# Kernel tuning notes

Measured on AMD Instinct MI355X. Metric: run time of the kernel, lower is better.

The kernel has to match this reference:

```python
import jax, jax.numpy as jnp
import numpy as np

AC_KERNEL = 5


def deconv(x, w, stride):
    """torch ConvTranspose2d(k=3, p=1, bias=False), stride 1 or 2 (output_padding=1).
    w has torch layout [Cin, Cout, kH, kW]."""
    wk = jnp.transpose(w, (1, 0, 2, 3))[:, :, ::-1, ::-1]  # OIHW, spatially flipped
    dn = ('NCHW', 'OIHW', 'NCHW')
    if stride == 1:
        return jax.lax.conv_general_dilated(x, wk, (1, 1), ((1, 1), (1, 1)), dimension_numbers=dn)
    # stride 2: dilate input, pad (k-1-p, k-1-p+op) = (1, 2) -> doubles H, W
    return jax.lax.conv_general_dilated(x, wk, (1, 1), ((1, 2), (1, 2)),
                                        lhs_dilation=(2, 2), dimension_numbers=dn)


def sepconv(feat, kv, kh, K):
    """Per-pixel adaptive separable convolution (Niklaus SepConv).
    feat: [B,C,H,W]; kv, kh: [B,K,H,W]. Replication-pad by K//2, then
    out[b,c,y,x] = sum_{i,j} pad[b,c,y+i,x+j] * kv[b,i,y,x] * kh[b,j,y,x]."""
    pad = K // 2
    B, C, H, W = feat.shape
    p = jnp.pad(feat, ((0, 0), (0, 0), (pad, pad), (pad, pad)), mode='edge')
    out = jnp.zeros_like(feat)
    for i in range(K):  # small fixed loop over kernel taps
        row = p[:, :, i:i + H, :]  # [B,C,H,W+2*pad]
        horiz = row[:, :, :, 0:W] * kh[:, 0:1]
        for j in range(1, K):
            horiz = horiz + row[:, :, :, j:j + W] * kh[:, j:j + 1]
        out = out + kv[:, i:i + 1] * horiz
    return out


def fusion(feat, kv, kh, mask):
    tmp = sepconv(feat, kv, kh, AC_KERNEL)
    return mask * tmp + (1.0 - mask) * feat


def setup_inputs() -> dict:
    key = jax.random.key(0)
    ks = jax.random.split(key, 20)
    B, G = 128, 64
    d = {'cont_feat': jax.random.normal(ks[0], (B, G, 8, 8), jnp.float32)}
    sizes = [8, 16, 32, 64]
    for li, s in enumerate(sizes):
        d[f'kv{li}'] = jax.random.uniform(ks[1 + 3 * li], (B, AC_KERNEL, s, s), jnp.float32)
        d[f'kh{li}'] = jax.random.uniform(ks[2 + 3 * li], (B, AC_KERNEL, s, s), jnp.float32)
        d[f'm{li}'] = jax.random.uniform(ks[3 + 3 * li], (B, 1, s, s), jnp.float32)
    wshapes = [(G, G * 8, 3, 3), (G * 8, G * 4, 3, 3), (G * 4, G * 2, 3, 3),
               (G * 2, G * 2, 3, 3), (G * 2, G, 3, 3), (G, 3, 3, 3)]
    for wi, ws in enumerate(wshapes):
        d[f'w{wi + 1}'] = jax.random.normal(ks[13 + wi], ws, jnp.float32) * 0.05
    return d


def reference(cont_feat, kv0, kh0, m0, kv1, kh1, m1, kv2, kh2, m2, kv3, kh3, m3,
              w1, w2, w3, w4, w5, w6):
    # kernel_layer = 4, no_mask = False, use_bn = False
    feat_8 = fusion(cont_feat, kv0, kh0, m0)                      # [B,G,8,8]
    feat_16 = jax.nn.relu(deconv(feat_8, w1, 2))                  # [B,8G,16,16]
    feat_16 = fusion(feat_16, kv1, kh1, m1)
    h = jax.nn.relu(deconv(feat_16, w2, 1))                       # [B,4G,16,16]
    feat_32 = jax.nn.relu(deconv(h, w3, 2))                       # [B,2G,32,32]
    feat_32 = fusion(feat_32, kv2, kh2, m2)
    h = jax.nn.relu(deconv(feat_32, w4, 1))                       # [B,2G,32,32]
    h = jax.nn.relu(deconv(h, w5, 2))                             # [B,G,64,64]
    out = jnp.tanh(deconv(h, w6, 1))                              # [B,3,64,64]
    out = fusion(out, kv3, kh3, m3)
    return (out, feat_8, feat_16, feat_32)
```

## Files before the change

kernel.cpp:

```cpp
#include <hip/hip_runtime.h>
#include <math.h>

typedef short v8s __attribute__((ext_vector_type(8)));
typedef float v16f __attribute__((ext_vector_type(16)));

__device__ inline unsigned short f2bf(float f) {
    union { float f; unsigned u; } c; c.f = f;
    unsigned r = (c.u + 0x7fffu + ((c.u >> 16) & 1u)) >> 16;
    return (unsigned short)r;
}

__global__ __launch_bounds__(256) void fusion_kernel(
        const float* __restrict__ feat, const float* __restrict__ kv,
        const float* __restrict__ kh, const float* __restrict__ m,
        float* __restrict__ out, int C, int H, int W, int total) {
    int idx = blockIdx.x * 256 + threadIdx.x;
    if (idx >= total) return;
    int x = idx % W;
    int y = (idx / W) % H;
    int b = idx / (W * H * C);
    int hw = H * W;
    int pix = y * W + x;
    float mv = m[b * hw + pix];
    float kvv[5], khv[5];
#pragma unroll
    for (int i = 0; i < 5; i++) {
        kvv[i] = kv[(b * 5 + i) * hw + pix];
        khv[i] = kh[(b * 5 + i) * hw + pix];
    }
    int cx[5], cy[5];
#pragma unroll
    for (int j = 0; j < 5; j++) {
        int xx = x + j - 2; cx[j] = xx < 0 ? 0 : (xx >= W ? W - 1 : xx);
        int yy = y + j - 2; cy[j] = yy < 0 ? 0 : (yy >= H ? H - 1 : yy);
    }
    const float* fp = feat + (size_t)(idx - pix);
    float s = 0.f;
#pragma unroll
    for (int i = 0; i < 5; i++) {
        const float* rp = fp + cy[i] * W;
        float h = 0.f;
#pragma unroll
        for (int j = 0; j < 5; j++) h += rp[cx[j]] * khv[j];
        s += kvv[i] * h;
    }
    float fv = feat[idx];
    out[idx] = mv * s + (1.f - mv) * fv;
}

__global__ __launch_bounds__(256) void nchw_to_nhwc_bf16(
        const float* __restrict__ in, unsigned short* __restrict__ out,
        int C, int H, int W, int lw, int lc2) {
    extern __shared__ unsigned short sm_t[];
    const int y = blockIdx.x, b = blockIdx.y;
    const int Cp = C + 8;
    const int tid = threadIdx.x;
    for (int i = tid; i < C * W; i += 256) {
        int x = i & (W - 1), c = i >> lw;
        float v = in[(((size_t)b * C + c) * H + y) * W + x];
        sm_t[x * Cp + c] = f2bf(v);
    }
    __syncthreads();
    const unsigned* s32 = (const unsigned*)sm_t;
    unsigned* o32 = (unsigned*)(out + (((size_t)b * H + y) * W) * C);
    const int n32 = (W * C) >> 1;
    for (int i = tid; i < n32; i += 256) {
        int x = i >> lc2;
        int c2 = i - (x << lc2);
        o32[i] = s32[x * (Cp >> 1) + c2];
    }
}

__global__ __launch_bounds__(256) void repack_w_frag(
        const float* __restrict__ w, unsigned short* __restrict__ wk,
        int Cin, int Cout, int flip) {
    int idx = blockIdx.x * 256 + threadIdx.x;
    if (idx >= Cin * Cout) return;
    int ci = idx / Cout, co = idx - ci * Cout;
    const float* src = w + (size_t)idx * 9;
    const int nCb = Cout >> 5, nH = Cin >> 4;
    const size_t inner = (size_t)((((ci >> 3) & 1) * 32 + (co & 31)) * 8 + (ci & 7));
#pragma unroll
    for (int k = 0; k < 9; k++) {
        int t = flip ? (8 - k) : k;
        size_t blk = ((size_t)t * nCb + (co >> 5)) * nH + (ci >> 4);
        wk[(blk << 9) + inner] = f2bf(src[k]);
    }
}

template<int W, int TH, int LW>
__global__ __launch_bounds__(256) void conv3x3_mfma(
        const unsigned short* __restrict__ X,
        const unsigned short* __restrict__ Wk,
        unsigned short* __restrict__ out, int Cin, int Cout, int H) {
    constexpr int TP = (TH + 2) * (W + 2);
    __shared__ unsigned short sB[TP * 40];
    const int tid = threadIdx.x;
    const int lane = tid & 63, wv = tid >> 6;
    const int wm = wv >> 1, wn = wv & 1;
    const int y0 = blockIdx.x * TH;
    const int coB = blockIdx.y * 128 + wm * 64;
    const int b = blockIdx.z;
    const int n = lane & 31, kg = lane >> 5;
    const int p0 = wn * 64 + n, p1 = p0 + 32;
    const int r0 = p0 >> LW, c0 = p0 & (W - 1);
    const int r1 = p1 >> LW, c1 = p1 & (W - 1);
    const int bo0 = (r0 * (W + 2) + c0) * 40 + kg * 8;
    const int bo1 = (r1 * (W + 2) + c1) * 40 + kg * 8;
    v16f acc00 = {}, acc01 = {}, acc10 = {}, acc11 = {};
    const size_t cbStride = (size_t)(Cin >> 4) << 9;
    const size_t tStride  = (size_t)(Cout >> 5) * cbStride;
    const unsigned short* Af = Wk + (size_t)(coB >> 5) * cbStride + (lane << 3);
    const unsigned short* Xb = X + (size_t)b * H * W * Cin;

    for (int ci0 = 0; ci0 < Cin; ci0 += 32) {
        for (int i = tid; i < TP * 4; i += 256) {
            int pix = i >> 2, part = i & 3;
            int py = pix / (W + 2), px = pix - py * (W + 2);
            int gy = y0 + py - 1, gx = px - 1;
            uint4 v = make_uint4(0u, 0u, 0u, 0u);
            if (gy >= 0 && gy < H && (unsigned)gx < (unsigned)W)
                v = *(const uint4*)(Xb + ((size_t)(gy * W + gx)) * Cin + ci0 + part * 8);
            *(uint4*)(sB + pix * 40 + part * 8) = v;
        }
        __syncthreads();
#pragma unroll
        for (int t = 0; t < 9; t++) {
            const int ky = t / 3, kx = t - ky * 3;
            const int toff = (ky * (W + 2) + kx) * 40;
#pragma unroll
            for (int kh = 0; kh < 2; kh++) {
                const unsigned short* ap =
                    Af + (size_t)t * tStride + (size_t)(((ci0 >> 4) + kh) << 9);
                v8s A0 = *(const v8s*)(ap);
                v8s A1 = *(const v8s*)(ap + cbStride);
                v8s B0 = *(const v8s*)(sB + bo0 + toff + kh * 16);
                v8s B1 = *(const v8s*)(sB + bo1 + toff + kh * 16);
                acc00 = __builtin_amdgcn_mfma_f32_32x32x16_bf16(A0, B0, acc00, 0, 0, 0);
                acc01 = __builtin_amdgcn_mfma_f32_32x32x16_bf16(A0, B1, acc01, 0, 0, 0);
                acc10 = __builtin_amdgcn_mfma_f32_32x32x16_bf16(A1, B0, acc10, 0, 0, 0);
                acc11 = __builtin_amdgcn_mfma_f32_32x32x16_bf16(A1, B1, acc11, 0, 0, 0);
            }
        }
        __syncthreads();
    }
    unsigned short* ob = out + (size_t)b * H * W * Cout;
#pragma unroll
    for (int sm = 0; sm < 2; sm++) {
        v16f a0 = sm ? acc10 : acc00;
        v16f a1 = sm ? acc11 : acc01;
        const int cobase = coB + sm * 32 + 4 * kg;
        unsigned short* q0p = ob + ((size_t)((y0 + r0) * W + c0)) * Cout + cobase;
        unsigned short* q1p = ob + ((size_t)((y0 + r1) * W + c1)) * Cout + cobase;
#pragma unroll
        for (int r2 = 0; r2 < 4; r2++) {
            ushort4 q0, q1; float v;
            v = a0[4 * r2 + 0]; v = v > 0.f ? v : 0.f; q0.x = f2bf(v);
            v = a0[4 * r2 + 1]; v = v > 0.f ? v : 0.f; q0.y = f2bf(v);
            v = a0[4 * r2 + 2]; v = v > 0.f ? v : 0.f; q0.z = f2bf(v);
            v = a0[4 * r2 + 3]; v = v > 0.f ? v : 0.f; q0.w = f2bf(v);
            *(ushort4*)(q0p + 8 * r2) = q0;
            v = a1[4 * r2 + 0]; v = v > 0.f ? v : 0.f; q1.x = f2bf(v);
            v = a1[4 * r2 + 1]; v = v > 0.f ? v : 0.f; q1.y = f2bf(v);
            v = a1[4 * r2 + 2]; v = v > 0.f ? v : 0.f; q1.z = f2bf(v);
            v = a1[4 * r2 + 3]; v = v > 0.f ? v : 0.f; q1.w = f2bf(v);
            *(ushort4*)(q1p + 8 * r2) = q1;
        }
    }
}

template<int W, int TH, int NWN, int NWM, int LW>
__global__ __launch_bounds__(256) void deconv2_mfma(
        const unsigned short* __restrict__ X,
        const unsigned short* __restrict__ Wk,
        float* __restrict__ out, int Cin, int Cout, int Hin) {
    constexpr int ROWS = NWN * TH + 1;
    constexpr int NPIX = ROWS * (W + 1);
    __shared__ unsigned short sB[NPIX * 40];
    const int tid = threadIdx.x;
    const int lane = tid & 63, wv = tid >> 6;
    const int wm = wv / NWN, wn = wv % NWN;
    const int n = lane & 31, kg = lane >> 5;
    const int y0 = blockIdx.x * (NWN * TH);
    const int coB = (blockIdx.y * NWM + wm) * 64;
    const int b = blockIdx.z;
    const int Yl = wn * TH + (n >> LW);
    const int Xl = n & (W - 1);
    v16f zero = {};
    v16f acc[2][2][2];
#pragma unroll
    for (int i = 0; i < 2; i++)
#pragma unroll
        for (int j = 0; j < 2; j++)
#pragma unroll
            for (int s = 0; s < 2; s++) acc[i][j][s] = zero;
    const unsigned short* Xb = X + (size_t)b * Hin * W * Cin;
    const size_t cbStride = (size_t)(Cin >> 4) << 9;
    const size_t tStride  = (size_t)(Cout >> 5) * cbStride;
    const unsigned short* Af = Wk + (size_t)(coB >> 5) * cbStride + (lane << 3);
    const int PY[3] = {1, 0, 1}, DY[3] = {1, 0, 0};

    for (int ci0 = 0; ci0 < Cin; ci0 += 32) {
        for (int i = tid; i < NPIX * 4; i += 256) {
            int pix = i >> 2, part = i & 3;
            int py_ = pix / (W + 1), px_ = pix - py_ * (W + 1);
            int gy = y0 + py_, gx = px_;
            uint4 v = make_uint4(0u, 0u, 0u, 0u);
            if (gy < Hin && gx < W)
                v = *(const uint4*)(Xb + ((size_t)(gy * W + gx)) * Cin + ci0 + part * 8);
            *(uint4*)(sB + pix * 40 + part * 8) = v;
        }
        __syncthreads();
#pragma unroll
        for (int ky = 0; ky < 3; ky++) {
#pragma unroll
            for (int kx = 0; kx < 3; kx++) {
                const int py = PY[ky], dy = DY[ky];
                const int px = PY[kx], dx = DY[kx];
                const int t = ky * 3 + kx;
                const int boff = ((Yl + dy) * (W + 1) + (Xl + dx)) * 40 + kg * 8;
#pragma unroll
                for (int kh = 0; kh < 2; kh++) {
                    const unsigned short* ap =
                        Af + (size_t)t * tStride + (size_t)(((ci0 >> 4) + kh) << 9);
                    v8s B  = *(const v8s*)(sB + boff + kh * 16);
                    v8s A0 = *(const v8s*)(ap);
                    v8s A1 = *(const v8s*)(ap + cbStride);
                    acc[py][px][0] = __builtin_amdgcn_mfma_f32_32x32x16_bf16(A0, B, acc[py][px][0], 0, 0, 0);
                    acc[py][px][1] = __builtin_amdgcn_mfma_f32_32x32x16_bf16(A1, B, acc[py][px][1], 0, 0, 0);
                }
            }
        }
        __syncthreads();
    }
    const int Wo = 2 * W, Ho = 2 * Hin;
    const int yin = y0 + Yl;
#pragma unroll
    for (int py = 0; py < 2; py++) {
        const int oy = 2 * yin + py;
#pragma unroll
        for (int sm = 0; sm < 2; sm++) {
            const int cobase = coB + sm * 32 + 4 * kg;
#pragma unroll
            for (int r = 0; r < 16; r++) {
                int co = cobase + (r & 3) + 8 * (r >> 2);
                float v0 = acc[py][0][sm][r]; v0 = v0 > 0.f ? v0 : 0.f;
                float v1 = acc[py][1][sm][r]; v1 = v1 > 0.f ? v1 : 0.f;
                *(float2*)(out + (((size_t)(b * Cout + co) * Ho + oy) * Wo + 2 * Xl)) =
                    make_float2(v0, v1);
            }
        }
    }
}

__global__ __launch_bounds__(256) void conv_s1_c3_tanh_kernel(
        const float* __restrict__ in, const float* __restrict__ w,
        float* __restrict__ out, int Cin, int H, int W) {
    __shared__ float sIn[8][18][19];
    __shared__ float sW[8][3][9];
    const int tid = threadIdx.x;
    const int r = tid >> 4, c = tid & 15;
    const int ntx = W >> 4;
    const int tx0 = (blockIdx.x % ntx) << 4, ty0 = (blockIdx.x / ntx) << 4;
    const int b = blockIdx.z;
    const int hw = H * W;
    float acc[3] = {0.f, 0.f, 0.f};
    for (int ci0 = 0; ci0 < Cin; ci0 += 8) {
        for (int i = tid; i < 8 * 18 * 18; i += 256) {
            int ci = i / 324, rr = i % 324, ly = rr / 18, lx = rr % 18;
            int gy = ty0 + ly - 1, gx = tx0 + lx - 1;
            float v = 0.f;
            if (gy >= 0 && gy < H && gx >= 0 && gx < W)
                v = in[(size_t)(b * Cin + ci0 + ci) * hw + gy * W + gx];
            sIn[ci][ly][lx] = v;
        }
        for (int i = tid; i < 8 * 3 * 9; i += 256) {
            int ci = i / 27, rr = i % 27, co = rr / 9, k = rr % 9;
            sW[ci][co][k] = w[(size_t)((ci0 + ci) * 3 + co) * 9 + (8 - k)];
        }
        __syncthreads();
#pragma unroll
        for (int ci = 0; ci < 8; ci++) {
            float v00 = sIn[ci][r][c],     v01 = sIn[ci][r][c + 1],     v02 = sIn[ci][r][c + 2];
            float v10 = sIn[ci][r + 1][c], v11 = sIn[ci][r + 1][c + 1], v12 = sIn[ci][r + 1][c + 2];
            float v20 = sIn[ci][r + 2][c], v21 = sIn[ci][r + 2][c + 1], v22 = sIn[ci][r + 2][c + 2];
#pragma unroll
            for (int co = 0; co < 3; co++) {
                const float* wp = &sW[ci][co][0];
                acc[co] += v00 * wp[0] + v01 * wp[1] + v02 * wp[2]
                         + v10 * wp[3] + v11 * wp[4] + v12 * wp[5]
                         + v20 * wp[6] + v21 * wp[7] + v22 * wp[8];
            }
        }
        __syncthreads();
    }
#pragma unroll
    for (int co = 0; co < 3; co++)
        out[(size_t)(b * 3 + co) * hw + (ty0 + r) * W + tx0 + c] = tanhf(acc[co]);
}

extern "C" void kernel_launch(void* const* d_in, const int* in_sizes, int n_in,
                              void* d_out, int out_size, void* d_ws, size_t ws_size,
                              hipStream_t stream) {
    const float* cont = (const float*)d_in[0];
    const float* kv0 = (const float*)d_in[1];
    const float* kh0 = (const float*)d_in[2];
    const float* m0  = (const float*)d_in[3];
    const float* kv1 = (const float*)d_in[4];
    const float* kh1 = (const float*)d_in[5];
    const float* m1  = (const float*)d_in[6];
    const float* kv2 = (const float*)d_in[7];
    const float* kh2 = (const float*)d_in[8];
    const float* m2  = (const float*)d_in[9];
    const float* kv3 = (const float*)d_in[10];
    const float* kh3 = (const float*)d_in[11];
    const float* m3  = (const float*)d_in[12];
    const float* w1  = (const float*)d_in[13];
    const float* w2  = (const float*)d_in[14];
    const float* w3  = (const float*)d_in[15];
    const float* w4  = (const float*)d_in[16];
    const float* w5  = (const float*)d_in[17];
    const float* w6  = (const float*)d_in[18];

    float* out = (float*)d_out;
    float* f8  = out + 1572864;
    float* f16 = out + 2097152;
    float* f32 = out + 18874368;

    char* ws = (char*)d_ws;

    float* A0 = (float*)ws;
    unsigned short* X8  = (unsigned short*)(ws + 67108864);
    unsigned short* Wk1 = (unsigned short*)(ws + 68157440);

    fusion_kernel<<<2048, 256, 0, stream>>>(cont, kv0, kh0, m0, f8, 64, 8, 8, 524288);
    nchw_to_nhwc_bf16<<<dim3(8, 128), 256, 8 * 72 * 2, stream>>>(f8, X8, 64, 8, 8, 3, 5);
    repack_w_frag<<<128, 256, 0, stream>>>(w1, Wk1, 64, 512, 0);
    deconv2_mfma<8, 4, 2, 2, 3><<<dim3(1, 4, 128), 256, 0, stream>>>(
        X8, Wk1, A0, 64, 512, 8);
    fusion_kernel<<<65536, 256, 0, stream>>>(A0, kv1, kh1, m1, f16, 512, 16, 16, 16777216);

    unsigned short* X16 = (unsigned short*)ws;
    unsigned short* h1b = (unsigned short*)(ws + 67108864);
    unsigned short* Wk3 = (unsigned short*)(ws + 83886080);
    unsigned short* Wk2 = (unsigned short*)(ws + 84475904);
    nchw_to_nhwc_bf16<<<dim3(16, 128), 256, 16 * 520 * 2, stream>>>(
        f16, X16, 512, 16, 16, 4, 8);
    repack_w_frag<<<512, 256, 0, stream>>>(w2, Wk2, 512, 256, 1);
    conv3x3_mfma<16, 8, 4><<<dim3(2, 2, 128), 256, 0, stream>>>(
        X16, Wk2, h1b, 512, 256, 16);
    repack_w_frag<<<128, 256, 0, stream>>>(w3, Wk3, 256, 128, 0);
    float* t32 = (float*)ws;
    deconv2_mfma<16, 2, 2, 2, 4><<<dim3(4, 1, 128), 256, 0, stream>>>(
        h1b, Wk3, t32, 256, 128, 16);
    fusion_kernel<<<65536, 256, 0, stream>>>(t32, kv2, kh2, m2, f32, 128, 32, 32, 16777216);

    unsigned short* Wk4  = (unsigned short*)ws;
    unsigned short* Wk5  = (unsigned short*)(ws + 294912);
    unsigned short* X32q = (unsigned short*)(ws + 524288);
    unsigned short* h2b  = (unsigned short*)(ws + 8912896);
    float* h3q = (float*)(ws + 17301504);
    float* tq  = (float*)(ws + 50855936);
    repack_w_frag<<<64, 256, 0, stream>>>(w4, Wk4, 128, 128, 1);
    repack_w_frag<<<32, 256, 0, stream>>>(w5, Wk5, 128, 64, 0);
    for (int q = 0; q < 4; q++) {
        size_t bo = (size_t)q * 32;
        const float* f32q = f32 + bo * 128 * 1024;
        nchw_to_nhwc_bf16<<<dim3(32, 32), 256, 32 * 136 * 2, stream>>>(
            f32q, X32q, 128, 32, 32, 5, 6);
        conv3x3_mfma<32, 4, 5><<<dim3(8, 1, 32), 256, 0, stream>>>(
            X32q, Wk4, h2b, 128, 128, 32);
        deconv2_mfma<32, 1, 4, 1, 5><<<dim3(8, 1, 32), 256, 0, stream>>>(
            h2b, Wk5, h3q, 128, 64, 32);
        conv_s1_c3_tanh_kernel<<<dim3(16, 1, 32), 256, 0, stream>>>(h3q, w6, tq, 64, 64, 64);
        fusion_kernel<<<1536, 256, 0, stream>>>(
            tq, kv3 + bo * 5 * 4096, kh3 + bo * 5 * 4096, m3 + bo * 4096,
            out + bo * 3 * 4096, 3, 64, 64, 393216);
    }
}
```

Baseline: 1.111 ms.

## Restructure fusion kernel to loop channels per thread and share rows via ds_bpermute

Each fusion thread now keeps its pixel's kv/kh/mask values in registers and walks a chunk of channels, so those per-pixel kernel weights are read once per chunk instead of once per channel. Horizontal neighbours come from other lanes' loaded values through ds_bpermute, which relies on a whole image row fitting in one 64-lane wavefront. This removes 20 of the 25 global loads per output and the index division and modulo work. The grid is now 2D over pixels and channel chunks, which gives less parallelism per thread but far more reuse.

```diff
diff --git a/kernel.cpp b/kernel.cpp
--- a/kernel.cpp
+++ b/kernel.cpp
@@ -10,42 +10,68 @@
     return (unsigned short)r;
 }
 
-__global__ __launch_bounds__(256) void fusion_kernel(
+template<int LW>
+__global__ __launch_bounds__(256) void fusion2_kernel(
         const float* __restrict__ feat, const float* __restrict__ kv,
         const float* __restrict__ kh, const float* __restrict__ m,
-        float* __restrict__ out, int C, int H, int W, int total) {
-    int idx = blockIdx.x * 256 + threadIdx.x;
-    if (idx >= total) return;
-    int x = idx % W;
-    int y = (idx / W) % H;
-    int b = idx / (W * H * C);
-    int hw = H * W;
-    int pix = y * W + x;
-    float mv = m[b * hw + pix];
+        float* __restrict__ out, int C, int CH, int H, int lhw) {
+    constexpr int W = 1 << LW;
+    const int t = blockIdx.x * 256 + threadIdx.x;
+    const int hw = H << LW;
+    const int b = t >> lhw;
+    const int pix = t & (hw - 1);
+    const int x = pix & (W - 1);
+    const int y = pix >> LW;
+    const int lane = threadIdx.x & 63;
+    const int rowbase = (lane & ~(W - 1)) << 2;
+
+    const int c0 = blockIdx.y * CH;
+
+    const float mv = m[(size_t)b * hw + pix];
     float kvv[5], khv[5];
 #pragma unroll
     for (int i = 0; i < 5; i++) {
-        kvv[i] = kv[(b * 5 + i) * hw + pix];
-        khv[i] = kh[(b * 5 + i) * hw + pix];
-    }
-    int cx[5], cy[5];
+        kvv[i] = kv[((size_t)b * 5 + i) * hw + pix];
+        khv[i] = kh[((size_t)b * 5 + i) * hw + pix];
+    }
+    int idx[5];
 #pragma unroll
     for (int j = 0; j < 5; j++) {
-        int xx = x + j - 2; cx[j] = xx < 0 ? 0 : (xx >= W ? W - 1 : xx);
-        int yy = y + j - 2; cy[j] = yy < 0 ? 0 : (yy >= H ? H - 1 : yy);
-    }
-    const float* fp = feat + (size_t)(idx - pix);
-    float s = 0.f;
+        int xx = x + j - 2; xx = xx < 0 ? 0 : (xx >= W ? W - 1 : xx);
+        idx[j] = rowbase + (xx << 2);
+    }
+    int roff[5];
 #pragma unroll
     for (int i = 0; i < 5; i++) {
-        const float* rp = fp + cy[i] * W;
-        float h = 0.f;
-#pragma unroll
-        for (int j = 0; j < 5; j++) h += rp[cx[j]] * khv[j];
-        s += kvv[i] * h;
-    }
-    float fv = feat[idx];
-    out[idx] = mv * s + (1.f - mv) * fv;
+        int yy = y + i - 2; yy = yy < 0 ? 0 : (yy >= H ? H - 1 : yy);
+        roff[i] = (yy << LW) + x;
+    }
+
+    const float* fbase = feat + ((size_t)b * C + c0) * hw;
+    float* obase = out + ((size_t)b * C + c0) * hw + pix;
+    const float om = 1.f - mv;
+
+#pragma unroll 4
+    for (int cc = 0; cc < CH; cc++) {
+        const float* q = fbase + (size_t)cc * hw;
+        float s = 0.f;
+        float fv = 0.f;
+#pragma unroll
+        for (int i = 0; i < 5; i++) {
+            float v = q[roff[i]];
+            if (i == 2) fv = v;
+            int vb = __float_as_int(v);
+            float h = 0.f;
+#pragma unroll
+            for (int j = 0; j < 5; j++) {
+                float nv = __int_as_float(
+                    __builtin_amdgcn_ds_bpermute(idx[j], vb));
+                h += nv * khv[j];
+            }
+            s += kvv[i] * h;
+        }
+        obase[(size_t)cc * hw] = mv * s + om * fv;
+    }
 }
 
 __global__ __launch_bounds__(256) void nchw_to_nhwc_bf16(
@@ -333,12 +359,14 @@
     unsigned short* X8  = (unsigned short*)(ws + 67108864);
     unsigned short* Wk1 = (unsigned short*)(ws + 68157440);
 
-    fusion_kernel<<<2048, 256, 0, stream>>>(cont, kv0, kh0, m0, f8, 64, 8, 8, 524288);
+    fusion2_kernel<3><<<dim3(32, 4), 256, 0, stream>>>(
+        cont, kv0, kh0, m0, f8, 64, 16, 8, 6);
     nchw_to_nhwc_bf16<<<dim3(8, 128), 256, 8 * 72 * 2, stream>>>(f8, X8, 64, 8, 8, 3, 5);
     repack_w_frag<<<128, 256, 0, stream>>>(w1, Wk1, 64, 512, 0);
     deconv2_mfma<8, 4, 2, 2, 3><<<dim3(1, 4, 128), 256, 0, stream>>>(
         X8, Wk1, A0, 64, 512, 8);
-    fusion_kernel<<<65536, 256, 0, stream>>>(A0, kv1, kh1, m1, f16, 512, 16, 16, 16777216);
+    fusion2_kernel<4><<<dim3(128, 32), 256, 0, stream>>>(
+        A0, kv1, kh1, m1, f16, 512, 16, 16, 8);
 
     unsigned short* X16 = (unsigned short*)ws;
     unsigned short* h1b = (unsigned short*)(ws + 67108864);
@@ -353,7 +381,8 @@
     float* t32 = (float*)ws;
     deconv2_mfma<16, 2, 2, 2, 4><<<dim3(4, 1, 128), 256, 0, stream>>>(
         h1b, Wk3, t32, 256, 128, 16);
-    fusion_kernel<<<65536, 256, 0, stream>>>(t32, kv2, kh2, m2, f32, 128, 32, 32, 16777216);
+    fusion2_kernel<5><<<dim3(512, 8), 256, 0, stream>>>(
+        t32, kv2, kh2, m2, f32, 128, 16, 32, 10);
 
     unsigned short* Wk4  = (unsigned short*)ws;
     unsigned short* Wk5  = (unsigned short*)(ws + 294912);
@@ -373,8 +402,8 @@
         deconv2_mfma<32, 1, 4, 1, 5><<<dim3(8, 1, 32), 256, 0, stream>>>(
             h2b, Wk5, h3q, 128, 64, 32);
         conv_s1_c3_tanh_kernel<<<dim3(16, 1, 32), 256, 0, stream>>>(h3q, w6, tq, 64, 64, 64);
-        fusion_kernel<<<1536, 256, 0, stream>>>(
+        fusion2_kernel<6><<<dim3(512, 1), 256, 0, stream>>>(
             tq, kv3 + bo * 5 * 4096, kh3 + bo * 5 * 4096, m3 + bo * 4096,
-            out + bo * 3 * 4096, 3, 64, 64, 393216);
-    }
-}
+            out + bo * 3 * 4096, 3, 3, 64, 12);
+    }
+}
```

Result: faster. 1.059 ms (-4.7%).
